# Performance work log

Hardware: AMD Instinct MI355X
Metric: run time of the kernel (lower is better)

Reference implementation:

```python
import jax, jax.numpy as jnp
import numpy as np

POS_T = 0.7
NEG_T = 0.3
TOTAL = 256      # total_num_samples
MAX_POS = 128    # max_pos_samples
N_ANCH = 262144
N_GT = 256
IMG_H = 1024
IMG_W = 1024


def _make_boxes(key, n, img_h, img_w, min_sz, max_sz):
    # boxes in (y1, x1, y2, x2); some anchors will fall outside the image
    kc, ks = jax.random.split(key)
    cy = jax.random.uniform(kc, (n,)) * img_h
    cx = jax.random.uniform(jax.random.fold_in(kc, 1), (n,)) * img_w
    h = min_sz + jax.random.uniform(ks, (n,)) * (max_sz - min_sz)
    w = min_sz + jax.random.uniform(jax.random.fold_in(ks, 1), (n,)) * (max_sz - min_sz)
    return jnp.stack([cy - h / 2, cx - w / 2, cy + h / 2, cx + w / 2], axis=1).astype(jnp.float32)


def setup_inputs() -> dict:
    key = jax.random.key(0)
    ka, kg = jax.random.split(key)
    anchors = _make_boxes(ka, N_ANCH, IMG_H, IMG_W, 16.0, 512.0)
    gt_bboxes = _make_boxes(kg, N_GT, IMG_H, IMG_W, 32.0, 256.0)
    # keep gt boxes inside the image
    gt_bboxes = jnp.clip(gt_bboxes, 0.0, jnp.array([IMG_H, IMG_W, IMG_H, IMG_W], jnp.float32))
    return {"anchors": anchors, "gt_bboxes": gt_bboxes, "image_h": IMG_H, "image_w": IMG_W}


def _pairwise_iou(boxes_a, boxes_b):
    # boxes_a: [N,4], boxes_b: [M,4] in (y1,x1,y2,x2)
    a = boxes_a[:, None, :]   # [N,1,4]
    b = boxes_b[None, :, :]   # [1,M,4]
    ih = jnp.clip(jnp.minimum(a[..., 2], b[..., 2]) - jnp.maximum(a[..., 0], b[..., 0]), 0.0)
    iw = jnp.clip(jnp.minimum(a[..., 3], b[..., 3]) - jnp.maximum(a[..., 1], b[..., 1]), 0.0)
    inter = ih * iw                                                  # [N,M]
    area_a = (boxes_a[:, 2] - boxes_a[:, 0]) * (boxes_a[:, 3] - boxes_a[:, 1])
    area_b = (boxes_b[:, 2] - boxes_b[:, 0]) * (boxes_b[:, 3] - boxes_b[:, 1])
    union = area_a[:, None] + area_b[None, :] - inter
    return inter / jnp.maximum(union, 1e-8)


def _forward(anchors, gt_bboxes, image_h, image_w):
    n = anchors.shape[0]
    # 1. boundary filter (kept as a mask -> fixed shapes, same semantics:
    #    out-of-image anchors get label -1 and are never sampled)
    inside = ((anchors[:, 0] >= 0) & (anchors[:, 1] >= 0) &
              (anchors[:, 2] <= image_h) & (anchors[:, 3] <= image_w))
    # 2. pairwise IoU   [N, M]
    iou = _pairwise_iou(anchors, gt_bboxes)
    max_ious = jnp.max(iou, axis=1)
    argmax_ious = jnp.argmax(iou, axis=1).astype(jnp.int32)
    # 3. threshold labeling
    labels = jnp.full((n,), -1, jnp.int32)
    labels = jnp.where(max_ious > POS_T, 1, labels)
    labels = jnp.where(max_ious < NEG_T, 0, labels)
    labels = jnp.where(inside, labels, -1)
    pos_mask = labels == 1
    neg_mask = labels == 0
    total_pos = jnp.sum(pos_mask.astype(jnp.int32))
    total_neg = jnp.sum(neg_mask.astype(jnp.int32))
    cur_pos = jnp.minimum(total_pos, MAX_POS)
    cur_neg = jnp.minimum(TOTAL - cur_pos, total_neg)
    # 5. random sampling via random-score top_k (fixed-shape analogue of
    #    tf.random_shuffle + slice)
    kp, kn = jax.random.split(jax.random.key(42))
    pos_scores = jnp.where(pos_mask, jax.random.uniform(kp, (n,)), -1.0)
    neg_scores = jnp.where(neg_mask, jax.random.uniform(kn, (n,)), -1.0)
    _, pos_idx = jax.lax.top_k(pos_scores, MAX_POS)   # original anchor ids
    _, neg_idx = jax.lax.top_k(neg_scores, TOTAL)
    # pack: first cur_pos slots are positives, next cur_neg are negatives,
    # remaining slots padded with -1 (original returns a dynamic-size concat)
    out_idx = jnp.full((TOTAL,), -1, jnp.int32)
    pslot = jnp.where(jnp.arange(MAX_POS) < cur_pos, jnp.arange(MAX_POS), TOTAL)
    out_idx = out_idx.at[pslot].set(pos_idx.astype(jnp.int32), mode='drop')
    nslot = jnp.where(jnp.arange(TOTAL) < cur_neg, cur_pos + jnp.arange(TOTAL), TOTAL)
    out_idx = out_idx.at[nslot].set(neg_idx.astype(jnp.int32), mode='drop')
    safe = jnp.clip(out_idx, 0, n - 1)
    valid = out_idx >= 0
    sel_labels = jnp.where(valid, labels[safe], -1)
    sel_gt = jnp.where(valid, argmax_ious[safe], -1)
    return out_idx, sel_labels, sel_gt, cur_pos


def reference(anchors, gt_bboxes, image_h, image_w):
    return _forward(anchors, gt_bboxes, image_h, image_w)
```

## Files before the change

### kernel.cpp

```cpp
#include <hip/hip_runtime.h>

#pragma clang fp contract(off)

#define N_ANCH   262144
#define N_GT     256
#define MAX_POSK 128
#define TOTALK   256
#define NBINS    2048
#define CAP      2048
#define BORDCAP  2048
#define CAP_P    32768
#define CAP_N    4096
#define T_N      2032

struct TF2 { unsigned a, b; };

__host__ __device__ constexpr unsigned rotl32(unsigned v, int d) {
  return (v << d) | (v >> (32 - d));
}

__host__ __device__ constexpr TF2 tf2x32(unsigned k0, unsigned k1,
                                         unsigned x0, unsigned x1) {
  unsigned ks2 = k0 ^ k1 ^ 0x1BD11BDAu;
  x0 += k0; x1 += k1;
  x0 += x1; x1 = rotl32(x1, 13); x1 ^= x0;
  x0 += x1; x1 = rotl32(x1, 15); x1 ^= x0;
  x0 += x1; x1 = rotl32(x1, 26); x1 ^= x0;
  x0 += x1; x1 = rotl32(x1,  6); x1 ^= x0;
  x0 += k1; x1 += ks2 + 1u;
  x0 += x1; x1 = rotl32(x1, 17); x1 ^= x0;
  x0 += x1; x1 = rotl32(x1, 29); x1 ^= x0;
  x0 += x1; x1 = rotl32(x1, 16); x1 ^= x0;
  x0 += x1; x1 = rotl32(x1, 24); x1 ^= x0;
  x0 += ks2; x1 += k0 + 2u;
  x0 += x1; x1 = rotl32(x1, 13); x1 ^= x0;
  x0 += x1; x1 = rotl32(x1, 15); x1 ^= x0;
  x0 += x1; x1 = rotl32(x1, 26); x1 ^= x0;
  x0 += x1; x1 = rotl32(x1,  6); x1 ^= x0;
  x0 += k0; x1 += k1 + 3u;
  x0 += x1; x1 = rotl32(x1, 17); x1 ^= x0;
  x0 += x1; x1 = rotl32(x1, 29); x1 ^= x0;
  x0 += x1; x1 = rotl32(x1, 16); x1 ^= x0;
  x0 += x1; x1 = rotl32(x1, 24); x1 ^= x0;
  x0 += k1; x1 += ks2 + 4u;
  x0 += x1; x1 = rotl32(x1, 13); x1 ^= x0;
  x0 += x1; x1 = rotl32(x1, 15); x1 ^= x0;
  x0 += x1; x1 = rotl32(x1, 26); x1 ^= x0;
  x0 += x1; x1 = rotl32(x1,  6); x1 ^= x0;
  x0 += ks2; x1 += k0 + 5u;
  return TF2{x0, x1};
}

constexpr unsigned KP0 = tf2x32(0u, 42u, 0u, 0u).a;
constexpr unsigned KP1 = tf2x32(0u, 42u, 0u, 0u).b;
constexpr unsigned KN0 = tf2x32(0u, 42u, 0u, 1u).a;
constexpr unsigned KN1 = tf2x32(0u, 42u, 0u, 1u).b;

__device__ inline unsigned score_bits(unsigned k0, unsigned k1, unsigned i) {
  TF2 r = tf2x32(k0, k1, 0u, i);
  return r.a ^ r.b;
}

constexpr double MPOSD = (double)0.7f + 0x1p-25;
constexpr double MNEGD = (double)0.3f - 0x1p-26;
constexpr float CPF = (float)(MPOSD / (1.0 + MPOSD));
constexpr float CNF = (float)(MNEGD / (1.0 + MNEGD));

__device__ unsigned g_packed[N_ANCH];
__device__ int      g_hist[2][NBINS];
__device__ int      g_nbord;
__device__ int      g_bord[BORDCAP];
__device__ int      g_cntp, g_cntn;
__device__ int      g_cand_p[CAP_P];
__device__ int      g_cand_n[CAP_N];

__device__ inline void finish_anchor(int i, float4 a, float mp, float mn,
                                     float Hf, float Wf) {
  const float A = (a.z - a.x) * (a.w - a.y);
  const float mrp = mp - CPF * A;
  const float mrn = mn - CNF * A;
  const bool inside = (a.x >= 0.0f) && (a.y >= 0.0f) && (a.z <= Hf) && (a.w <= Wf);
  const float band = 0x1.8p-21f * (A + 65536.0f);
  const bool pos = mrp > band;
  const bool nny = mrn > band;
  int lab = pos ? 1 : (nny ? -1 : 0);
  if (!inside) lab = -1;

  unsigned sb = 0u;
  if (lab >= 0) {
    sb = score_bits(lab == 1 ? KP0 : KN0, lab == 1 ? KP1 : KN1, (unsigned)i);
    atomicAdd(&g_hist[lab == 1 ? 0 : 1][sb >> 21], 1);
    if (lab == 1) {
      int q = atomicAdd(&g_cntp, 1);
      if (q < CAP_P) g_cand_p[q] = i;
    } else if ((sb >> 21) >= T_N) {
      int q = atomicAdd(&g_cntn, 1);
      if (q < CAP_N) g_cand_n[q] = i;
    }
  }
  g_packed[i] = (sb & ~511u) | (unsigned)(lab + 1);

  if (inside && (fabsf(mrp) <= band || fabsf(mrn) <= band)) {
    int b = atomicAdd(&g_nbord, 1);
    if (b < BORDCAP) g_bord[b] = i;
  }
}

__global__ __launch_bounds__(256) void k_main(const float4* __restrict__ anchors,
                                              const float4* __restrict__ gt,
                                              const int* __restrict__ ph,
                                              const int* __restrict__ pw) {
  __shared__ float4 s_gt[N_GT];
  __shared__ float2 s_tpn[N_GT];
  const int tid = threadIdx.x;
  {
    float4 g = gt[tid];
    s_gt[tid] = g;
    float B = (g.z - g.x) * (g.w - g.y);
    s_tpn[tid] = make_float2(CPF * B, CNF * B);
  }
  __syncthreads();

  const int i = blockIdx.x * 256 + tid;
  const float4 a = anchors[i];
  const float Hf = (float)(*ph);
  const float Wf = (float)(*pw);

  float mpA = -1e30f, mnA = -1e30f, mpB = -1e30f, mnB = -1e30f;
  #pragma unroll 8
  for (int j = 0; j < N_GT; j += 2) {
    {
      const float4 b = s_gt[j];
      const float2 t = s_tpn[j];
      float ih = fmaxf(fminf(a.z, b.z) - fmaxf(a.x, b.x), 0.0f);
      float iw = fmaxf(fminf(a.w, b.w) - fmaxf(a.y, b.y), 0.0f);
      float in0 = ih * iw;
      mpA = fmaxf(mpA, in0 - t.x);
      mnA = fmaxf(mnA, in0 - t.y);
    }
    {
      const float4 b = s_gt[j + 1];
      const float2 t = s_tpn[j + 1];
      float ih = fmaxf(fminf(a.z, b.z) - fmaxf(a.x, b.x), 0.0f);
      float iw = fmaxf(fminf(a.w, b.w) - fmaxf(a.y, b.y), 0.0f);
      float in1 = ih * iw;
      mpB = fmaxf(mpB, in1 - t.x);
      mnB = fmaxf(mnB, in1 - t.y);
    }
  }
  finish_anchor(i, a, fmaxf(mpA, mpB), fmaxf(mnA, mnB), Hf, Wf);
}

__device__ inline unsigned long long shfl_xor_u64(unsigned long long v, int m) {
  unsigned lo = (unsigned)v, hi = (unsigned)(v >> 32);
  lo = __shfl_xor(lo, m, 64);
  hi = __shfl_xor(hi, m, 64);
  return ((unsigned long long)hi << 32) | lo;
}

__global__ __launch_bounds__(1024) void k_tail(const float4* __restrict__ anchors,
                                               const float4* __restrict__ gt,
                                               int* __restrict__ out) {
  __shared__ unsigned long long s_keys[2][CAP];
  __shared__ int    s_hist[2][NBINS];
  __shared__ float4 s_gt[N_GT];
  __shared__ int    s_cs[2][128];
  __shared__ int    s_sx[2][128];
  __shared__ int    s_sel[TOTALK];
  __shared__ int    s_cut[2], s_cnt[2], s_cur[2], s_full;
  const int tid  = threadIdx.x;
  const int wid  = tid >> 6, lane = tid & 63;

  for (int t = tid; t < N_GT; t += 1024) s_gt[t] = gt[t];
  for (int t = tid; t < 2 * NBINS; t += 1024)
    (&s_hist[0][0])[t] = (&g_hist[0][0])[t];
  if (tid < 2) s_cnt[tid] = 0;
  __syncthreads();

  int nb = g_nbord; if (nb > BORDCAP) nb = BORDCAP;
  for (int b = wid; b < nb; b += 16) {
    const int i = g_bord[b];
    const float4 a = anchors[i];
    const float A = (a.z - a.x) * (a.w - a.y);
    bool p = false, nn = false;
    #pragma unroll
    for (int k = 0; k < 4; ++k) {
      const int j = lane + 64 * k;
      float4 bb = s_gt[j];
      float ih = fmaxf(fminf(a.z, bb.z) - fmaxf(a.x, bb.x), 0.0f);
      float iw = fmaxf(fminf(a.w, bb.w) - fmaxf(a.y, bb.y), 0.0f);
      float inter = ih * iw;
      float Bar = (bb.z - bb.x) * (bb.w - bb.y);
      float uni = (A + Bar) - inter;
      double id = (double)inter, ud = (double)uni;
      p  |= (id >= MPOSD * ud);
      nn |= (id >= MNEGD * ud);
    }
    unsigned long long bp = __ballot(p);
    unsigned long long bn = __ballot(nn);
    if (lane == 0) {
      int newlab = bp ? 1 : (bn ? -1 : 0);
      unsigned old = g_packed[i];
      int oldlab = (int)(old & 3u) - 1;
      if (newlab != oldlab) {
        if (oldlab >= 0) atomicAdd(&s_hist[oldlab == 1 ? 0 : 1][old >> 21], -1);
        unsigned sb = 0u;
        if (newlab >= 0) {
          sb = score_bits(newlab == 1 ? KP0 : KN0, newlab == 1 ? KP1 : KN1, (unsigned)i);
          atomicAdd(&s_hist[newlab == 1 ? 0 : 1][sb >> 21], 1);
          if (newlab == 1) {
            int q = atomicAdd(&g_cntp, 1);
            if (q < CAP_P) g_cand_p[q] = i;
          } else if ((sb >> 21) >= T_N) {
            int q = atomicAdd(&g_cntn, 1);
            if (q < CAP_N) g_cand_n[q] = i;
          }
        }
        g_packed[i] = (sb & ~511u) | (unsigned)(newlab + 1);
      }
    }
  }
  __syncthreads();

  if (tid < 256) {
    const int cls = tid >> 7, c = tid & 127;
    int s = 0;
    #pragma unroll
    for (int b = c * 16; b < c * 16 + 16; ++b) s += s_hist[cls][b];
    s_cs[cls][c] = s;
  }
  __syncthreads();
  if (tid < 256) {
    const int cls = tid >> 7, c = tid & 127;
    int s = 0;
    for (int c2 = c + 1; c2 < 128; ++c2) s += s_cs[cls][c2];
    s_sx[cls][c] = s;
  }
  __syncthreads();
  if (tid == 0) {
    int total_p = s_sx[0][0] + s_cs[0][0];
    int total_n = s_sx[1][0] + s_cs[1][0];
    int cur_pos = total_p < MAX_POSK ? total_p : MAX_POSK;
    int rem = TOTALK - cur_pos;
    int cur_neg = total_n < rem ? total_n : rem;
    s_cur[0] = cur_pos;
    s_cur[1] = cur_neg;
    s_cut[0] = NBINS;
    s_cut[1] = NBINS;
  }
  __syncthreads();
  if (tid < 256) {
    const int cls = tid >> 7, c = tid & 127;
    const int K = s_cur[cls];
    if (K > 0) {
      const int sx = s_sx[cls][c];
      if (sx < K && sx + s_cs[cls][c] >= K) {
        int suffix = sx;
        int cut = c * 16;
        for (int b = c * 16 + 15; b >= c * 16; --b) {
          suffix += s_hist[cls][b];
          if (suffix >= K) { cut = b; break; }
        }
        s_cut[cls] = cut;
      }
    }
  }
  __syncthreads();
  if (tid == 0) {
    s_full = (g_cntp > CAP_P) || (g_cntn > CAP_N) ||
             (s_cur[1] > 0 && s_cut[1] < T_N);
  }
  __syncthreads();

  const int cut0 = s_cut[0], cut1 = s_cut[1];
  if (!s_full) {
    int Cp = g_cntp;
    for (int t = tid; t < Cp; t += 1024) {
      const int i = g_cand_p[t];
      const unsigned p = g_packed[i];
      if ((p & 3u) == 2u && (int)(p >> 21) >= cut0) {
        int q = atomicAdd(&s_cnt[0], 1);
        if (q < CAP)
          s_keys[0][q] = ((unsigned long long)(p >> 9) << 32) | (unsigned)(~i);
      }
    }
    int Cn = g_cntn;
    for (int t = tid; t < Cn; t += 1024) {
      const int i = g_cand_n[t];
      const unsigned p = g_packed[i];
      if ((p & 3u) == 1u && (int)(p >> 21) >= cut1) {
        int q = atomicAdd(&s_cnt[1], 1);
        if (q < CAP)
          s_keys[1][q] = ((unsigned long long)(p >> 9) << 32) | (unsigned)(~i);
      }
    }
  } else {
    for (int i = tid; i < N_ANCH; i += 1024) {
      const unsigned p = g_packed[i];
      const int lab0 = (int)(p & 3u);
      if (lab0 == 0) continue;
      const int s = (lab0 == 2) ? 0 : 1;
      if ((int)(p >> 21) >= (s == 0 ? cut0 : cut1)) {
        int q = atomicAdd(&s_cnt[s], 1);
        if (q < CAP)
          s_keys[s][q] = ((unsigned long long)(p >> 9) << 32) | (unsigned)(~i);
      }
    }
  }
  for (int t = tid; t < TOTALK; t += 1024) s_sel[t] = -1;
  for (int t = tid; t < 3 * TOTALK; t += 1024) out[t] = -1;
  __syncthreads();

  const int cur_pos = s_cur[0], cur_neg = s_cur[1];
  if (tid == 0) out[3 * TOTALK] = cur_pos;
  int Cp = s_cnt[0]; if (Cp > CAP) Cp = CAP;
  int Cn = s_cnt[1]; if (Cn > CAP) Cn = CAP;
  for (int t = tid; t < Cp; t += 1024) {
    unsigned long long me = s_keys[0][t];
    int r = 0;
    for (int u = 0; u < Cp; ++u) r += (s_keys[0][u] > me);
    if (r < cur_pos) {
      int idx = (int)(~(unsigned)me);
      s_sel[r] = idx;
      out[r] = idx;
      out[TOTALK + r] = 1;
    }
  }
  for (int t = tid; t < Cn; t += 1024) {
    unsigned long long me = s_keys[1][t];
    int r = 0;
    for (int u = 0; u < Cn; ++u) r += (s_keys[1][u] > me);
    if (r < cur_neg) {
      int idx = (int)(~(unsigned)me);
      s_sel[cur_pos + r] = idx;
      out[cur_pos + r] = idx;
      out[TOTALK + cur_pos + r] = 0;
    }
  }
  __syncthreads();

  {
    const int slot = tid >> 2;
    const int q    = tid & 3;
    const int idx  = s_sel[slot];
    const int safe = idx < 0 ? 0 : idx;
    const float4 a = anchors[safe];
    const float A = (a.z - a.x) * (a.w - a.y);
    unsigned long long key = 0ULL;
    for (int k = 0; k < 64; ++k) {
      const int j = q * 64 + k;
      const float4 b = s_gt[j];
      const float B = (b.z - b.x) * (b.w - b.y);
      float ih = fmaxf(fminf(a.z, b.z) - fmaxf(a.x, b.x), 0.0f);
      float iw = fmaxf(fminf(a.w, b.w) - fmaxf(a.y, b.y), 0.0f);
      float inter = ih * iw;
      float uni = (A + B) - inter;
      float iou = inter / fmaxf(uni, 1e-8f);
      unsigned long long kk =
          ((unsigned long long)__float_as_uint(iou) << 32) | (unsigned)(~j);
      key = kk > key ? kk : key;
    }
    unsigned long long o1 = shfl_xor_u64(key, 1); key = o1 > key ? o1 : key;
    unsigned long long o2 = shfl_xor_u64(key, 2); key = o2 > key ? o2 : key;
    if (q == 0 && idx >= 0)
      out[2 * TOTALK + slot] = (int)(~(unsigned)key) & 0xFF;
  }
  __syncthreads();

  for (int t = tid; t < 2 * NBINS; t += 1024) (&g_hist[0][0])[t] = 0;
  if (tid == 0) { g_nbord = 0; g_cntp = 0; g_cntn = 0; }
}

extern "C" void kernel_launch(void* const* d_in, const int* in_sizes, int n_in,
                              void* d_out, int out_size, void* d_ws, size_t ws_size,
                              hipStream_t stream) {
  (void)in_sizes; (void)n_in; (void)out_size; (void)d_ws; (void)ws_size;
  const float4* anchors = (const float4*)d_in[0];
  const float4* gt      = (const float4*)d_in[1];
  const int*    ph      = (const int*)d_in[2];
  const int*    pw      = (const int*)d_in[3];
  int*          out     = (int*)d_out;

  k_main<<<N_ANCH / 256, 256, 0, stream>>>(anchors, gt, ph, pw);
  k_tail<<<1, 1024, 0, stream>>>(anchors, gt, out);
}
```

Measured before the change: 124.0 us.

## Read GT boxes from global memory in main loop; drop shared histogram copy in tail

In k_main, the GT boxes are now read through the cache from global memory (uniform addresses) instead of from LDS, and only the precomputed area thresholds stay in shared memory, packed two per float4. In k_tail, the shared histogram copy is removed: border updates apply atomics directly to the global histogram, and each scan thread keeps its 16 bins in registers for the cut search. The aim is less LDS traffic and a smaller LDS footprint, plus removing the histogram copy. In exchange it relies on scalar/cached global loads and uses global atomics in the border pass.

```diff
diff --git a/kernel.cpp b/kernel.cpp
--- a/kernel.cpp
+++ b/kernel.cpp
@@ -110,14 +110,14 @@
                                               const float4* __restrict__ gt,
                                               const int* __restrict__ ph,
                                               const int* __restrict__ pw) {
-  __shared__ float4 s_gt[N_GT];
-  __shared__ float2 s_tpn[N_GT];
+  __shared__ float4 s_tpn2[N_GT / 2];
   const int tid = threadIdx.x;
-  {
-    float4 g = gt[tid];
-    s_gt[tid] = g;
-    float B = (g.z - g.x) * (g.w - g.y);
-    s_tpn[tid] = make_float2(CPF * B, CNF * B);
+  if (tid < N_GT / 2) {
+    float4 g0 = gt[2 * tid];
+    float4 g1 = gt[2 * tid + 1];
+    float B0 = (g0.z - g0.x) * (g0.w - g0.y);
+    float B1 = (g1.z - g1.x) * (g1.w - g1.y);
+    s_tpn2[tid] = make_float4(CPF * B0, CNF * B0, CPF * B1, CNF * B1);
   }
   __syncthreads();
 
@@ -127,25 +127,24 @@
   const float Wf = (float)(*pw);
 
   float mpA = -1e30f, mnA = -1e30f, mpB = -1e30f, mnB = -1e30f;
-  #pragma unroll 8
-  for (int j = 0; j < N_GT; j += 2) {
+  #pragma unroll 4
+  for (int jp = 0; jp < N_GT / 2; ++jp) {
+    const float4 b0 = gt[2 * jp];
+    const float4 b1 = gt[2 * jp + 1];
+    const float4 t  = s_tpn2[jp];
     {
-      const float4 b = s_gt[j];
-      const float2 t = s_tpn[j];
-      float ih = fmaxf(fminf(a.z, b.z) - fmaxf(a.x, b.x), 0.0f);
-      float iw = fmaxf(fminf(a.w, b.w) - fmaxf(a.y, b.y), 0.0f);
+      float ih = fmaxf(fminf(a.z, b0.z) - fmaxf(a.x, b0.x), 0.0f);
+      float iw = fmaxf(fminf(a.w, b0.w) - fmaxf(a.y, b0.y), 0.0f);
       float in0 = ih * iw;
       mpA = fmaxf(mpA, in0 - t.x);
       mnA = fmaxf(mnA, in0 - t.y);
     }
     {
-      const float4 b = s_gt[j + 1];
-      const float2 t = s_tpn[j + 1];
-      float ih = fmaxf(fminf(a.z, b.z) - fmaxf(a.x, b.x), 0.0f);
-      float iw = fmaxf(fminf(a.w, b.w) - fmaxf(a.y, b.y), 0.0f);
+      float ih = fmaxf(fminf(a.z, b1.z) - fmaxf(a.x, b1.x), 0.0f);
+      float iw = fmaxf(fminf(a.w, b1.w) - fmaxf(a.y, b1.y), 0.0f);
       float in1 = ih * iw;
-      mpB = fmaxf(mpB, in1 - t.x);
-      mnB = fmaxf(mnB, in1 - t.y);
+      mpB = fmaxf(mpB, in1 - t.z);
+      mnB = fmaxf(mnB, in1 - t.w);
     }
   }
   finish_anchor(i, a, fmaxf(mpA, mpB), fmaxf(mnA, mnB), Hf, Wf);
@@ -162,7 +161,6 @@
                                                const float4* __restrict__ gt,
                                                int* __restrict__ out) {
   __shared__ unsigned long long s_keys[2][CAP];
-  __shared__ int    s_hist[2][NBINS];
   __shared__ float4 s_gt[N_GT];
   __shared__ int    s_cs[2][128];
   __shared__ int    s_sx[2][128];
@@ -172,8 +170,6 @@
   const int wid  = tid >> 6, lane = tid & 63;
 
   for (int t = tid; t < N_GT; t += 1024) s_gt[t] = gt[t];
-  for (int t = tid; t < 2 * NBINS; t += 1024)
-    (&s_hist[0][0])[t] = (&g_hist[0][0])[t];
   if (tid < 2) s_cnt[tid] = 0;
   __syncthreads();
 
@@ -203,11 +199,11 @@
       unsigned old = g_packed[i];
       int oldlab = (int)(old & 3u) - 1;
       if (newlab != oldlab) {
-        if (oldlab >= 0) atomicAdd(&s_hist[oldlab == 1 ? 0 : 1][old >> 21], -1);
+        if (oldlab >= 0) atomicAdd(&g_hist[oldlab == 1 ? 0 : 1][old >> 21], -1);
         unsigned sb = 0u;
         if (newlab >= 0) {
           sb = score_bits(newlab == 1 ? KP0 : KN0, newlab == 1 ? KP1 : KN1, (unsigned)i);
-          atomicAdd(&s_hist[newlab == 1 ? 0 : 1][sb >> 21], 1);
+          atomicAdd(&g_hist[newlab == 1 ? 0 : 1][sb >> 21], 1);
           if (newlab == 1) {
             int q = atomicAdd(&g_cntp, 1);
             if (q < CAP_P) g_cand_p[q] = i;
@@ -222,11 +218,12 @@
   }
   __syncthreads();
 
+  int h[16];
   if (tid < 256) {
     const int cls = tid >> 7, c = tid & 127;
     int s = 0;
     #pragma unroll
-    for (int b = c * 16; b < c * 16 + 16; ++b) s += s_hist[cls][b];
+    for (int k = 0; k < 16; ++k) { h[k] = g_hist[cls][c * 16 + k]; s += h[k]; }
     s_cs[cls][c] = s;
   }
   __syncthreads();
@@ -257,9 +254,10 @@
       if (sx < K && sx + s_cs[cls][c] >= K) {
         int suffix = sx;
         int cut = c * 16;
-        for (int b = c * 16 + 15; b >= c * 16; --b) {
-          suffix += s_hist[cls][b];
-          if (suffix >= K) { cut = b; break; }
+        #pragma unroll
+        for (int k = 15; k >= 0; --k) {
+          suffix += h[k];
+          if (suffix >= K) { cut = c * 16 + k; break; }
         }
         s_cut[cls] = cut;
       }
```

New measurement: 117.9 us. 1.05x faster.
